# Kernel tuning notes

Hardware: AMD Instinct MI355X
Metric: run time of the kernel (lower is better)

The kernel has to match this reference:

```python
import jax, jax.numpy as jnp
import numpy as np

T, B, I, H = 4096, 2048, 1, 10


def setup_inputs() -> dict:
    key = jax.random.key(0)
    ks = jax.random.split(key, 8)
    k = 1.0 / np.sqrt(H)  # torch default init bound for RNN and Linear(10,1)
    u = lambda kk, shape: jax.random.uniform(kk, shape, jnp.float32, -k, k)
    return {
        "x": jax.random.normal(ks[0], (T, B, I), jnp.float32),
        "h": jnp.zeros((1, B, H), jnp.float32),
        "W_ih": u(ks[1], (H, I)),
        "b_ih": u(ks[2], (H,)),
        "W_hh": u(ks[3], (H, H)),
        "b_hh": u(ks[4], (H,)),
        "W_out": u(ks[5], (1, H)),
        "b_out": u(ks[6], (1,)),
    }


def reference(x, h, W_ih, b_ih, W_hh, b_hh, W_out, b_out):
    # Vanilla RNN: h_t = tanh(x_t @ W_ih^T + b_ih + h_{t-1} @ W_hh^T + b_hh)
    b = b_ih + b_hh  # fuse the two biases once

    def step(h_prev, x_t):  # h_prev: [B,H], x_t: [B,I]
        h_new = jnp.tanh(x_t @ W_ih.T + h_prev @ W_hh.T + b)
        return h_new, h_new

    h_last, ys = jax.lax.scan(step, h[0], x)  # ys: [T,B,H]
    out = ys @ W_out.T + b_out  # [T,B,1]
    return out, h_last[None]  # h: [1,B,H]
```

## Files before the change

### kernel.cpp

```cpp
#include <hip/hip_runtime.h>

#define T_STEPS 4096
#define BATCH   2048
#define HID     10
#define UB      16

__device__ __forceinline__ void issue16(float (&xr)[UB], const float* base) {
#pragma unroll
    for (int u = 0; u < UB; ++u)
        asm volatile("global_load_dword %0, %1, off"
                     : "=v"(xr[u]) : "v"(base + (size_t)u * BATCH) : "memory");
}
#define BIND16(a) "+v"(a[0]),"+v"(a[1]),"+v"(a[2]),"+v"(a[3]),"+v"(a[4]), \
    "+v"(a[5]),"+v"(a[6]),"+v"(a[7]),"+v"(a[8]),"+v"(a[9]),"+v"(a[10]),   \
    "+v"(a[11]),"+v"(a[12]),"+v"(a[13]),"+v"(a[14]),"+v"(a[15])
__device__ __forceinline__ void wait1_bind(float (&xr)[UB]) {
    asm volatile("s_waitcnt vmcnt(1)" : BIND16(xr) :: "memory");
}
__device__ __forceinline__ void wait0_bind(float (&xr)[UB]) {
    asm volatile("s_waitcnt vmcnt(0)" : BIND16(xr) :: "memory");
}

__device__ __forceinline__ void step_blob(float& h, float& p, float& pk,
                                          float x, float wih, float bj,
                                          float wo, float m,
                                          const float (&w)[16]) {
    float c0, c1;
    asm volatile(
        "v_fma_f32 %[c0], %[wih], %[x], %[bj]\n\t"
        "v_mul_f32_dpp %[c1], %[h], %[w4] row_ror:4 row_mask:0xf bank_mask:0xf\n\t"
        "v_add_f32_dpp %[p], %[p], %[p] row_ror:8 row_mask:0xf bank_mask:0xf\n\t"
        "v_fmac_f32 %[c0], %[h], %[w0]\n\t"
        "v_fmac_f32_dpp %[c0], %[h], %[w1] row_ror:1 row_mask:0xf bank_mask:0xf\n\t"
        "v_add_f32_dpp %[p], %[p], %[p] row_ror:4 row_mask:0xf bank_mask:0xf\n\t"
        "v_fmac_f32_dpp %[c1], %[h], %[w5] row_ror:5 row_mask:0xf bank_mask:0xf\n\t"
        "v_fmac_f32_dpp %[c0], %[h], %[w2] row_ror:2 row_mask:0xf bank_mask:0xf\n\t"
        "v_add_f32_dpp %[p], %[p], %[p] row_ror:2 row_mask:0xf bank_mask:0xf\n\t"
        "v_fmac_f32_dpp %[c1], %[h], %[w6] row_ror:6 row_mask:0xf bank_mask:0xf\n\t"
        "v_fmac_f32_dpp %[c0], %[h], %[w3] row_ror:3 row_mask:0xf bank_mask:0xf\n\t"
        "v_add_f32_dpp %[p], %[p], %[p] row_ror:1 row_mask:0xf bank_mask:0xf\n\t"
        "v_fmac_f32_dpp %[c1], %[h], %[w7] row_ror:7 row_mask:0xf bank_mask:0xf\n\t"
        "v_fmac_f32_dpp %[c0], %[h], %[w8] row_ror:8 row_mask:0xf bank_mask:0xf\n\t"
        "v_fmac_f32 %[pk], %[p], %[m]\n\t"
        "v_fmac_f32_dpp %[c1], %[h], %[w9] row_ror:9 row_mask:0xf bank_mask:0xf\n\t"
        "v_fmac_f32_dpp %[c0], %[h], %[w10] row_ror:10 row_mask:0xf bank_mask:0xf\n\t"
        "v_fmac_f32_dpp %[c1], %[h], %[w11] row_ror:11 row_mask:0xf bank_mask:0xf\n\t"
        "v_fmac_f32_dpp %[c0], %[h], %[w12] row_ror:12 row_mask:0xf bank_mask:0xf\n\t"
        "v_fmac_f32_dpp %[c1], %[h], %[w13] row_ror:13 row_mask:0xf bank_mask:0xf\n\t"
        "v_fmac_f32_dpp %[c0], %[h], %[w14] row_ror:14 row_mask:0xf bank_mask:0xf\n\t"
        "v_fmac_f32_dpp %[c1], %[h], %[w15] row_ror:15 row_mask:0xf bank_mask:0xf\n\t"
        "v_add_f32 %[c0], %[c0], %[c1]\n\t"
        "v_mul_f32 %[c0], 0x4038aa3b, %[c0]\n\t"
        "v_exp_f32 %[c0], %[c0]\n\t"
        "s_nop 0\n\t"
        "v_add_f32 %[c0], 1.0, %[c0]\n\t"
        "v_rcp_f32 %[c0], %[c0]\n\t"
        "s_nop 0\n\t"
        "v_fma_f32 %[h], -2.0, %[c0], 1.0\n\t"
        "v_mul_f32 %[p], %[wo], %[h]"
        : [c0]"=&v"(c0), [c1]"=&v"(c1), [h]"+v"(h), [p]"+v"(p), [pk]"+v"(pk)
        : [x]"v"(x), [wih]"v"(wih), [bj]"v"(bj), [wo]"v"(wo), [m]"v"(m),
          [w0]"v"(w[0]),  [w1]"v"(w[1]),  [w2]"v"(w[2]),  [w3]"v"(w[3]),
          [w4]"v"(w[4]),  [w5]"v"(w[5]),  [w6]"v"(w[6]),  [w7]"v"(w[7]),
          [w8]"v"(w[8]),  [w9]"v"(w[9]),  [w10]"v"(w[10]),[w11]"v"(w[11]),
          [w12]"v"(w[12]),[w13]"v"(w[13]),[w14]"v"(w[14]),[w15]"v"(w[15]));
}

__device__ __forceinline__ void finish_reduce(float& p, float& pk, float m15) {
    asm volatile(
        "s_nop 1\n\t"
        "v_add_f32_dpp %[p], %[p], %[p] row_ror:8 row_mask:0xf bank_mask:0xf\n\t"
        "s_nop 1\n\t"
        "v_add_f32_dpp %[p], %[p], %[p] row_ror:4 row_mask:0xf bank_mask:0xf\n\t"
        "s_nop 1\n\t"
        "v_add_f32_dpp %[p], %[p], %[p] row_ror:2 row_mask:0xf bank_mask:0xf\n\t"
        "s_nop 1\n\t"
        "v_add_f32_dpp %[p], %[p], %[p] row_ror:1 row_mask:0xf bank_mask:0xf\n\t"
        "v_fmac_f32 %[pk], %[p], %[m]"
        : [p]"+v"(p), [pk]"+v"(pk)
        : [m]"v"(m15));
}

__global__ __launch_bounds__(64, 1) void rnn_kernel(
    const float* __restrict__ x,
    const float* __restrict__ h0,
    const float* __restrict__ W_ih,
    const float* __restrict__ b_ih,
    const float* __restrict__ W_hh,
    const float* __restrict__ b_hh,
    const float* __restrict__ W_out,
    const float* __restrict__ b_out,
    float* __restrict__ out)
{
    const int tid = threadIdx.x;
    const int j   = tid & 15;
    const int b   = (blockIdx.x << 2) + (tid >> 4);
    const bool jv = (j < HID);
    const int jc  = jv ? j : 0;

    const float wih  = jv ? W_ih[jc] : 0.0f;
    const float bj   = jv ? (b_ih[jc] + b_hh[jc]) : 0.0f;
    const float wo_j = jv ? W_out[jc] : 0.0f;
    const float bo   = b_out[0];

    float wsh[16];
#pragma unroll
    for (int N = 0; N < 16; ++N) {
        const int k = (j - N) & 15;
        wsh[N] = (jv && k < HID) ? W_hh[jc * HID + k] : 0.0f;
    }

    float km[16];
#pragma unroll
    for (int i = 0; i < 16; ++i) km[i] = (j == i) ? 1.0f : 0.0f;
    const float mzero = 0.0f;

    float hval = jv ? h0[b * HID + jc] : 0.0f;
    float p = 0.0f, pk = 0.0f;

    const float* xb = x + b;
    float xA[UB], xB[UB];

    issue16(xA, xb);
    wait0_bind(xA);

    for (int t0 = 0; t0 < T_STEPS; t0 += 2 * UB) {
        wait1_bind(xA);
        issue16(xB, xb + (size_t)(t0 + UB) * BATCH);
#pragma unroll
        for (int u = 0; u < UB; ++u)
            step_blob(hval, p, pk, xA[u], wih, bj, wo_j,
                      (u == 0) ? mzero : km[u - 1], wsh);
        finish_reduce(p, pk, km[15]);
        out[(size_t)(t0 + j) * BATCH + b] = pk + bo;
        pk = 0.0f;

        wait1_bind(xB);
        const float* xsrc = (t0 + 2 * UB < T_STEPS)
                          ? (xb + (size_t)(t0 + 2 * UB) * BATCH) : xb;
        issue16(xA, xsrc);
#pragma unroll
        for (int u = 0; u < UB; ++u)
            step_blob(hval, p, pk, xB[u], wih, bj, wo_j,
                      (u == 0) ? mzero : km[u - 1], wsh);
        finish_reduce(p, pk, km[15]);
        out[(size_t)(t0 + UB + j) * BATCH + b] = pk + bo;
        pk = 0.0f;
    }

    wait0_bind(xA);

    if (jv) out[(size_t)T_STEPS * BATCH + (size_t)b * HID + j] = hval;
}

extern "C" void kernel_launch(void* const* d_in, const int* in_sizes, int n_in,
                              void* d_out, int out_size, void* d_ws, size_t ws_size,
                              hipStream_t stream) {
    const float* x     = (const float*)d_in[0];
    const float* h0    = (const float*)d_in[1];
    const float* W_ih  = (const float*)d_in[2];
    const float* b_ih  = (const float*)d_in[3];
    const float* W_hh  = (const float*)d_in[4];
    const float* b_hh  = (const float*)d_in[5];
    const float* W_out = (const float*)d_in[6];
    const float* b_out = (const float*)d_in[7];

    rnn_kernel<<<BATCH / 4, 64, 0, stream>>>(
        x, h0, W_ih, b_ih, W_hh, b_hh, W_out, b_out, (float*)d_out);
}
```

Measured before the change: 371.3 us.

## Carry reciprocal state r instead of h to shorten the recurrence critical path

Rewrites the recurrence in terms of r = 1/(1+exp(2z)), with h = 1 - 2r. The constant log2e scale and the -2 factor are folded into the precomputed weights, bias and output weights. This removes the scale multiply and the final FMA from the serial dependency chain of each step. The output projection moves to the start of the next step, and the final hidden state is rebuilt from r. It relies on exact algebraic folding with slightly different rounding, and adds a tail multiply plus an extra nop in the reduction.

Result: faster. 362.0 us (-2.5%).

```diff
diff --git a/kernel.cpp b/kernel.cpp
--- a/kernel.cpp
+++ b/kernel.cpp
@@ -21,53 +21,53 @@
     asm volatile("s_waitcnt vmcnt(0)" : BIND16(xr) :: "memory");
 }
 
-__device__ __forceinline__ void step_blob(float& h, float& p, float& pk,
-                                          float x, float wih, float bj,
-                                          float wo, float m,
+__device__ __forceinline__ void step_blob(float& r, float& p, float& pk,
+                                          float x, float wih2, float bj2,
+                                          float wo2, float m,
                                           const float (&w)[16]) {
     float c0, c1;
     asm volatile(
-        "v_fma_f32 %[c0], %[wih], %[x], %[bj]\n\t"
-        "v_mul_f32_dpp %[c1], %[h], %[w4] row_ror:4 row_mask:0xf bank_mask:0xf\n\t"
+        "v_fma_f32 %[c0], %[wih2], %[x], %[bj2]\n\t"
+        "v_mul_f32 %[p], %[wo2], %[r]\n\t"
+        "v_mul_f32_dpp %[c1], %[r], %[w4] row_ror:4 row_mask:0xf bank_mask:0xf\n\t"
+        "v_fmac_f32 %[c0], %[r], %[w0]\n\t"
+        "v_fmac_f32_dpp %[c1], %[r], %[w5] row_ror:5 row_mask:0xf bank_mask:0xf\n\t"
         "v_add_f32_dpp %[p], %[p], %[p] row_ror:8 row_mask:0xf bank_mask:0xf\n\t"
-        "v_fmac_f32 %[c0], %[h], %[w0]\n\t"
-        "v_fmac_f32_dpp %[c0], %[h], %[w1] row_ror:1 row_mask:0xf bank_mask:0xf\n\t"
+        "v_fmac_f32_dpp %[c0], %[r], %[w1] row_ror:1 row_mask:0xf bank_mask:0xf\n\t"
+        "v_fmac_f32_dpp %[c1], %[r], %[w6] row_ror:6 row_mask:0xf bank_mask:0xf\n\t"
         "v_add_f32_dpp %[p], %[p], %[p] row_ror:4 row_mask:0xf bank_mask:0xf\n\t"
-        "v_fmac_f32_dpp %[c1], %[h], %[w5] row_ror:5 row_mask:0xf bank_mask:0xf\n\t"
-        "v_fmac_f32_dpp %[c0], %[h], %[w2] row_ror:2 row_mask:0xf bank_mask:0xf\n\t"
+        "v_fmac_f32_dpp %[c0], %[r], %[w2] row_ror:2 row_mask:0xf bank_mask:0xf\n\t"
+        "v_fmac_f32_dpp %[c1], %[r], %[w7] row_ror:7 row_mask:0xf bank_mask:0xf\n\t"
         "v_add_f32_dpp %[p], %[p], %[p] row_ror:2 row_mask:0xf bank_mask:0xf\n\t"
-        "v_fmac_f32_dpp %[c1], %[h], %[w6] row_ror:6 row_mask:0xf bank_mask:0xf\n\t"
-        "v_fmac_f32_dpp %[c0], %[h], %[w3] row_ror:3 row_mask:0xf bank_mask:0xf\n\t"
+        "v_fmac_f32_dpp %[c0], %[r], %[w3] row_ror:3 row_mask:0xf bank_mask:0xf\n\t"
+        "v_fmac_f32_dpp %[c1], %[r], %[w8] row_ror:8 row_mask:0xf bank_mask:0xf\n\t"
         "v_add_f32_dpp %[p], %[p], %[p] row_ror:1 row_mask:0xf bank_mask:0xf\n\t"
-        "v_fmac_f32_dpp %[c1], %[h], %[w7] row_ror:7 row_mask:0xf bank_mask:0xf\n\t"
-        "v_fmac_f32_dpp %[c0], %[h], %[w8] row_ror:8 row_mask:0xf bank_mask:0xf\n\t"
+        "v_fmac_f32_dpp %[c0], %[r], %[w10] row_ror:10 row_mask:0xf bank_mask:0xf\n\t"
+        "v_fmac_f32_dpp %[c1], %[r], %[w9] row_ror:9 row_mask:0xf bank_mask:0xf\n\t"
         "v_fmac_f32 %[pk], %[p], %[m]\n\t"
-        "v_fmac_f32_dpp %[c1], %[h], %[w9] row_ror:9 row_mask:0xf bank_mask:0xf\n\t"
-        "v_fmac_f32_dpp %[c0], %[h], %[w10] row_ror:10 row_mask:0xf bank_mask:0xf\n\t"
-        "v_fmac_f32_dpp %[c1], %[h], %[w11] row_ror:11 row_mask:0xf bank_mask:0xf\n\t"
-        "v_fmac_f32_dpp %[c0], %[h], %[w12] row_ror:12 row_mask:0xf bank_mask:0xf\n\t"
-        "v_fmac_f32_dpp %[c1], %[h], %[w13] row_ror:13 row_mask:0xf bank_mask:0xf\n\t"
-        "v_fmac_f32_dpp %[c0], %[h], %[w14] row_ror:14 row_mask:0xf bank_mask:0xf\n\t"
-        "v_fmac_f32_dpp %[c1], %[h], %[w15] row_ror:15 row_mask:0xf bank_mask:0xf\n\t"
+        "v_fmac_f32_dpp %[c0], %[r], %[w12] row_ror:12 row_mask:0xf bank_mask:0xf\n\t"
+        "v_fmac_f32_dpp %[c1], %[r], %[w11] row_ror:11 row_mask:0xf bank_mask:0xf\n\t"
+        "v_fmac_f32_dpp %[c0], %[r], %[w14] row_ror:14 row_mask:0xf bank_mask:0xf\n\t"
+        "v_fmac_f32_dpp %[c1], %[r], %[w13] row_ror:13 row_mask:0xf bank_mask:0xf\n\t"
+        "v_fmac_f32_dpp %[c0], %[r], %[w15] row_ror:15 row_mask:0xf bank_mask:0xf\n\t"
         "v_add_f32 %[c0], %[c0], %[c1]\n\t"
-        "v_mul_f32 %[c0], 0x4038aa3b, %[c0]\n\t"
         "v_exp_f32 %[c0], %[c0]\n\t"
         "s_nop 0\n\t"
         "v_add_f32 %[c0], 1.0, %[c0]\n\t"
-        "v_rcp_f32 %[c0], %[c0]\n\t"
-        "s_nop 0\n\t"
-        "v_fma_f32 %[h], -2.0, %[c0], 1.0\n\t"
-        "v_mul_f32 %[p], %[wo], %[h]"
-        : [c0]"=&v"(c0), [c1]"=&v"(c1), [h]"+v"(h), [p]"+v"(p), [pk]"+v"(pk)
-        : [x]"v"(x), [wih]"v"(wih), [bj]"v"(bj), [wo]"v"(wo), [m]"v"(m),
+        "v_rcp_f32 %[r], %[c0]\n\t"
+        "s_nop 0"
+        : [c0]"=&v"(c0), [c1]"=&v"(c1), [r]"+v"(r), [p]"+v"(p), [pk]"+v"(pk)
+        : [x]"v"(x), [wih2]"v"(wih2), [bj2]"v"(bj2), [wo2]"v"(wo2), [m]"v"(m),
           [w0]"v"(w[0]),  [w1]"v"(w[1]),  [w2]"v"(w[2]),  [w3]"v"(w[3]),
           [w4]"v"(w[4]),  [w5]"v"(w[5]),  [w6]"v"(w[6]),  [w7]"v"(w[7]),
           [w8]"v"(w[8]),  [w9]"v"(w[9]),  [w10]"v"(w[10]),[w11]"v"(w[11]),
           [w12]"v"(w[12]),[w13]"v"(w[13]),[w14]"v"(w[14]),[w15]"v"(w[15]));
 }
 
-__device__ __forceinline__ void finish_reduce(float& p, float& pk, float m15) {
+__device__ __forceinline__ void finish_reduce(float r, float& p, float& pk,
+                                              float wo2, float m15) {
     asm volatile(
+        "v_mul_f32 %[p], %[wo2], %[r]\n\t"
         "s_nop 1\n\t"
         "v_add_f32_dpp %[p], %[p], %[p] row_ror:8 row_mask:0xf bank_mask:0xf\n\t"
         "s_nop 1\n\t"
@@ -76,9 +76,10 @@
         "v_add_f32_dpp %[p], %[p], %[p] row_ror:2 row_mask:0xf bank_mask:0xf\n\t"
         "s_nop 1\n\t"
         "v_add_f32_dpp %[p], %[p], %[p] row_ror:1 row_mask:0xf bank_mask:0xf\n\t"
+        "s_nop 1\n\t"
         "v_fmac_f32 %[pk], %[p], %[m]"
         : [p]"+v"(p), [pk]"+v"(pk)
-        : [m]"v"(m15));
+        : [r]"v"(r), [wo2]"v"(wo2), [m]"v"(m15));
 }
 
 __global__ __launch_bounds__(64, 1) void rnn_kernel(
@@ -98,24 +99,37 @@
     const bool jv = (j < HID);
     const int jc  = jv ? j : 0;
 
-    const float wih  = jv ? W_ih[jc] : 0.0f;
-    const float bj   = jv ? (b_ih[jc] + b_hh[jc]) : 0.0f;
-    const float wo_j = jv ? W_out[jc] : 0.0f;
-    const float bo   = b_out[0];
+    const float CC = 2.88539008177792681472f;
+
+    const float wih = jv ? W_ih[jc] : 0.0f;
+    const float bj  = jv ? (b_ih[jc] + b_hh[jc]) : 0.0f;
+    const float wo  = jv ? W_out[jc] : 0.0f;
 
     float wsh[16];
+    float wsum = 0.0f;
 #pragma unroll
     for (int N = 0; N < 16; ++N) {
         const int k = (j - N) & 15;
         wsh[N] = (jv && k < HID) ? W_hh[jc * HID + k] : 0.0f;
+        wsum += wsh[N];
     }
+
+    const float wih2 = CC * wih;
+    const float bj2  = CC * (bj + wsum);
+    float w2[16];
+#pragma unroll
+    for (int N = 0; N < 16; ++N) w2[N] = -2.0f * CC * wsh[N];
+    const float wo2 = -2.0f * wo;
+    float c0sum = b_out[0];
+#pragma unroll
+    for (int k = 0; k < HID; ++k) c0sum += W_out[k];
 
     float km[16];
 #pragma unroll
     for (int i = 0; i < 16; ++i) km[i] = (j == i) ? 1.0f : 0.0f;
     const float mzero = 0.0f;
 
-    float hval = jv ? h0[b * HID + jc] : 0.0f;
+    float rval = fmaf(-0.5f, jv ? h0[b * HID + jc] : 0.0f, 0.5f);
     float p = 0.0f, pk = 0.0f;
 
     const float* xb = x + b;
@@ -129,10 +143,10 @@
         issue16(xB, xb + (size_t)(t0 + UB) * BATCH);
 #pragma unroll
         for (int u = 0; u < UB; ++u)
-            step_blob(hval, p, pk, xA[u], wih, bj, wo_j,
-                      (u == 0) ? mzero : km[u - 1], wsh);
-        finish_reduce(p, pk, km[15]);
-        out[(size_t)(t0 + j) * BATCH + b] = pk + bo;
+            step_blob(rval, p, pk, xA[u], wih2, bj2, wo2,
+                      (u == 0) ? mzero : km[u - 1], w2);
+        finish_reduce(rval, p, pk, wo2, km[15]);
+        out[(size_t)(t0 + j) * BATCH + b] = pk + c0sum;
         pk = 0.0f;
 
         wait1_bind(xB);
@@ -141,16 +155,17 @@
         issue16(xA, xsrc);
 #pragma unroll
         for (int u = 0; u < UB; ++u)
-            step_blob(hval, p, pk, xB[u], wih, bj, wo_j,
-                      (u == 0) ? mzero : km[u - 1], wsh);
-        finish_reduce(p, pk, km[15]);
-        out[(size_t)(t0 + UB + j) * BATCH + b] = pk + bo;
+            step_blob(rval, p, pk, xB[u], wih2, bj2, wo2,
+                      (u == 0) ? mzero : km[u - 1], w2);
+        finish_reduce(rval, p, pk, wo2, km[15]);
+        out[(size_t)(t0 + UB + j) * BATCH + b] = pk + c0sum;
         pk = 0.0f;
     }
 
     wait0_bind(xA);
 
-    if (jv) out[(size_t)T_STEPS * BATCH + (size_t)b * HID + j] = hval;
+    if (jv) out[(size_t)T_STEPS * BATCH + (size_t)b * HID + j]
+                = fmaf(-2.0f, rval, 1.0f);
 }
 
 extern "C" void kernel_launch(void* const* d_in, const int* in_sizes, int n_in,
```
